# Performance work log

Measured on AMD Instinct MI355X. Metric: run time of the kernel, lower is better.

## Reference

```python
import jax
import jax.numpy as jnp
from jax import lax
import numpy as np

B, ND, H, W = 8, 8, 512, 512
CONF = 0.9
MARGIN = 3.0
MIN_CLUSTER = 50
MAX_X = 102.4
MPP0, MPP1 = 0.2, 0.2
K = 32  # max clusters (torch version grows an unbounded python list)


def setup_inputs() -> dict:
    key = jax.random.key(0)
    k1, k2, k3, k4, k5, k6 = jax.random.split(key, 6)
    return {
        "seg": jax.random.uniform(k1, (B, 1, H, W), dtype=jnp.float32),
        "embedding": jax.random.normal(k2, (B, ND, H, W), dtype=jnp.float32),
        "offset_pred": jax.random.normal(k3, (B, 1, H, W), dtype=jnp.float32),
        "z_pred": jax.random.normal(k4, (B, 1, H, W), dtype=jnp.float32),
        "intrinsic": jax.random.normal(k5, (B, 3, 3), dtype=jnp.float32),
        "extrinsic": jax.random.normal(k6, (B, 4, 4), dtype=jnp.float32),
    }


def _cluster_one(seg_flat, emb_flat):
    # seg_flat: [N], emb_flat: [N, ND]. Greedy sequential embedding clustering
    # (naive_cluster_nd): running-mean centers, assign to nearest center if
    # within MARGIN else open a new one. Fixed K slots; counts>0 marks active.
    nd = emb_flat.shape[1]

    def step(carry, xs):
        centers, counts = carry  # [K, nd], [K]
        s, e = xs
        valid = s >= CONF
        d = jnp.sqrt(jnp.sum((centers - e) ** 2, axis=1))
        d = jnp.where(counts > 0, d, jnp.inf)
        cid_min = jnp.argmin(d).astype(jnp.int32)
        join = d[cid_min] < MARGIN
        n_active = jnp.sum(counts > 0).astype(jnp.int32)
        cid = jnp.where(join, cid_min, jnp.minimum(n_active, K - 1))
        cnt = counts[cid]
        new_c = jnp.where(join, (centers[cid] * cnt + e) / (cnt + 1.0), e)
        centers = jnp.where(valid, centers.at[cid].set(new_c), centers)
        counts = jnp.where(valid, counts.at[cid].add(1.0), counts)
        return (centers, counts), jnp.where(valid, cid, -1)

    init = (jnp.zeros((K, nd), emb_flat.dtype), jnp.zeros((K,), emb_flat.dtype))
    (_, _), cids = lax.scan(step, init, (seg_flat, emb_flat))
    return cids  # [N] int32, -1 = background


def reference(seg, embedding, offset_pred, z_pred, intrinsic, extrinsic):
    b, nd, h, w = embedding.shape
    seg_flat = seg[:, 0].reshape(b, h * w)
    emb_flat = embedding.reshape(b, nd, h * w).transpose(0, 2, 1)  # [B, N, nd]
    cids = jax.vmap(_cluster_one)(seg_flat, emb_flat).reshape(b, h, w)
    lanes = jnp.where(cids >= 0, cids + 1, 0)  # [B, H, W], 0 = background

    # mean_col_by_row_with_offset_z: per (batch, lane, row) mean of col+offset and z
    offset_y = jax.nn.sigmoid(offset_pred[:, 0])          # [B, H, W]
    x_adj = jnp.arange(w, dtype=seg.dtype)[None, None, :] + offset_y
    zc = z_pred[:, 0]
    b_idx = jnp.arange(b)[:, None, None]
    h_idx = jnp.arange(h)[None, :, None]
    seg_ids = ((b_idx * (K + 1) + lanes) * h + h_idx).reshape(-1)
    num = b * (K + 1) * h

    def ssum(v):
        return jax.ops.segment_sum(v.reshape(-1), seg_ids, num_segments=num).reshape(b, K + 1, h)[:, 1:]

    cnt = ssum(jnp.ones((b, h, w), seg.dtype))            # [B, K, H]
    mean_x = ssum(x_adj) / jnp.maximum(cnt, 1.0)
    mean_z = ssum(zc) / jnp.maximum(cnt, 1.0)

    size = cnt.sum(-1)                                    # cluster pixel count
    n_rows = (cnt > 0).sum(-1)                            # rows per lane
    valid = (cnt > 0) & (size[:, :, None] >= MIN_CLUSTER) & (n_rows[:, :, None] >= 2)

    # ego-coordinate transform from forward()
    x_world = (MAX_X / MPP0 - (jnp.arange(h, dtype=seg.dtype) + 0.5)) * MPP0  # [H]
    x_world = jnp.broadcast_to(x_world, (b, K, h))
    y_world = -(mean_x - (w // 2)) * MPP1
    points = jnp.stack([x_world, y_world, mean_z], axis=1)  # [B, 3, K, H]
    points = jnp.where(valid[:, None], points, 0.0)
    return points, valid
```

## Files before the change

kernel.cpp:

```cpp
#include <hip/hip_runtime.h>

#define HW_ (512 * 512)
#define B_ 8
#define H_ 512
#define W_ 512
#define K_ 32
#define CH_ 16
#define CHPIX_ (HW_ / CH_)

typedef float float2v __attribute__((ext_vector_type(2)));

__global__ void k_count(const float* __restrict__ seg, int* __restrict__ chunkCnt) {
  const int blk = blockIdx.x;
  const int t = threadIdx.x;
  const float4* __restrict__ s4 = (const float4*)(seg + (size_t)blk * CHPIX_) + (size_t)t * 16;
  int cnt = 0;
#pragma unroll
  for (int j = 0; j < 16; ++j) {
    float4 v = s4[j];
    cnt += (v.x >= 0.9f) + (v.y >= 0.9f) + (v.z >= 0.9f) + (v.w >= 0.9f);
  }
  __shared__ int red[256];
  red[t] = cnt;
  __syncthreads();
  for (int off = 128; off > 0; off >>= 1) {
    if (t < off) red[t] += red[t + off];
    __syncthreads();
  }
  if (t == 0) chunkCnt[blk] = red[0];
}

__global__ void k_scan(const int* __restrict__ chunkCnt, int* __restrict__ chunkBase,
                       int* __restrict__ nvalid, int cap) {
  const int t = threadIdx.x;
  if (t < B_ * CH_) {
    const int b = t / CH_, c = t % CH_;
    int base = 0;
    for (int q = 0; q < c; ++q) base += chunkCnt[b * CH_ + q];
    chunkBase[t] = base;
    if (c == CH_ - 1) nvalid[b] = min(base + chunkCnt[t], cap);
  }
}

__global__ void k_fill(const float* __restrict__ seg, const float* __restrict__ emb,
                       const int* __restrict__ chunkBase, unsigned char* __restrict__ lanes,
                       int* __restrict__ idxC, float* __restrict__ embC, int cap) {
  const int blk = blockIdx.x;
  const int b = blk / CH_;
  const int t = threadIdx.x;
  const size_t pixbase = (size_t)blk * CHPIX_ + (size_t)t * 64;
  const float4* __restrict__ s4 = (const float4*)(seg + pixbase);

  int cnt = 0;
#pragma unroll
  for (int j = 0; j < 16; ++j) {
    float4 v = s4[j];
    cnt += (v.x >= 0.9f) + (v.y >= 0.9f) + (v.z >= 0.9f) + (v.w >= 0.9f);
  }
  __shared__ int pre[256];
  pre[t] = cnt;
  __syncthreads();
  for (int off = 1; off < 256; off <<= 1) {
    int mine = pre[t];
    int add = (t >= off) ? pre[t - off] : 0;
    __syncthreads();
    pre[t] = mine + add;
    __syncthreads();
  }
  int w = chunkBase[blk] + pre[t] - cnt;

  uint4 z = {0u, 0u, 0u, 0u};
  uint4* lz = (uint4*)(lanes + pixbase);
  lz[0] = z; lz[1] = z; lz[2] = z; lz[3] = z;

  const float* __restrict__ eb = emb + (size_t)b * 8 * HW_;
  const int pixInB = (int)(pixbase - (size_t)b * HW_);
  for (int j = 0; j < 16; ++j) {
    float4 v = s4[j];
    float sv[4] = {v.x, v.y, v.z, v.w};
#pragma unroll
    for (int q = 0; q < 4; ++q) {
      if (sv[q] >= 0.9f && w < cap) {
        const int p = pixInB + j * 4 + q;
        idxC[(size_t)b * cap + w] = p;
        float* dst = embC + ((size_t)b * cap + w) * 8;
#pragma unroll
        for (int dd = 0; dd < 8; ++dd) dst[dd] = eb[(size_t)dd * HW_ + p];
        ++w;
      }
    }
  }
}


#define TILE_ 32

__device__ __forceinline__ void stage16(const float* g, float* l) {
  __builtin_amdgcn_global_load_lds(
      (const __attribute__((address_space(1))) void*)g,
      (__attribute__((address_space(3))) void*)l, 16, 0, 0);
}

#define RLU(V, L) ((unsigned)__builtin_amdgcn_readlane((int)(V), (L)))
#define PKF(A, B, C) __builtin_elementwise_fma((A), (B), (C))

#define STEPQ(J, US, LS)                                                             \
  do {                                                                               \
    float2v t01 = C01 - e01_##US;                                                    \
    float2v t23 = C23 - e23_##US;                                                    \
    float2v t45 = C45 - e45_##US;                                                    \
    float2v t67 = C67 - e67_##US;                                                    \
    float2v p = t01 * t01;                                                           \
    p = PKF(t23, t23, p);                                                            \
    p = PKF(t45, t45, p);                                                            \
    p = PKF(t67, t67, p);                                                            \
    float dsq = p.x + p.y;                                                           \
    unsigned db = __float_as_uint(dsq);                                              \
    unsigned dbm = db > emptyBits ? db : emptyBits;         \
    unsigned mn = (dbm & 0xFFFFFFE0u) | (unsigned)cl;                                \
    unsigned mr;                                                                     \
    mr = (unsigned)__builtin_amdgcn_update_dpp(0, (int)mn, 0xB1, 0xF, 0xF, true);    \
    mn = mn < mr ? mn : mr;                                                          \
    mr = (unsigned)__builtin_amdgcn_update_dpp(0, (int)mn, 0x4E, 0xF, 0xF, true);    \
    mn = mn < mr ? mn : mr;                                                          \
    mr = (unsigned)__builtin_amdgcn_update_dpp(0, (int)mn, 0x141, 0xF, 0xF, true);   \
    mn = mn < mr ? mn : mr;                                                          \
    mr = (unsigned)__builtin_amdgcn_update_dpp(0, (int)mn, 0x140, 0xF, 0xF, true);   \
    mn = mn < mr ? mn : mr;                                                          \
    unsigned q0 = RLU(mn, 0), q1 = RLU(mn, 16);                                      \
    unsigned mv = q0 < q1 ? q0 : q1;                            \
    bool join = mv < 0x41100000u;            \
    int cid = join ? (int)(mv & 31u) : (nact < 31 ? nact : 31);                      \
    nact += join ? 0 : 1;                                                            \
    bool own = (cl == cid);                                                          \
    float wj = join ? inv : 1.0f;                                                    \
    float w = own ? wj : 0.0f;                                                       \
    float2v wv = {w, w};                                                             \
    C01 = PKF(t01, -wv, C01);                                          \
    C23 = PKF(t23, -wv, C23);                                                        \
    C45 = PKF(t45, -wv, C45);                                                        \
    C67 = PKF(t67, -wv, C67);                                                        \
    cnt += own ? 1.0f : 0.0f;                                                        \
    inv = __builtin_amdgcn_rcpf(cnt + 1.0f);          \
    emptyBits = own ? 0u : emptyBits;                                                \
    pk |= (unsigned long long)(unsigned)(cid + 1) << (((J) & 7) * 8);                \
    if (((J) & 7) == 7) {                                                            \
      if (lane == 0) *(unsigned long long*)(cptr + ((J) & ~7)) = pk;                 \
      pk = 0ULL;                                                                     \
    }                                                                                \
    if ((J) < TILE_ - 2) {       \
      e01_##LS = ebq[((J) + 2) * 4 + 0];                                             \
      e23_##LS = ebq[((J) + 2) * 4 + 1];                                             \
      e45_##LS = ebq[((J) + 2) * 4 + 2];                                             \
      e67_##LS = ebq[((J) + 2) * 4 + 3];                                             \
    }                                                                                \
  } while (0)

__global__ __launch_bounds__(64, 1) void k_cluster(const float* __restrict__ embC,
                                                   const int* __restrict__ nvalid,
                                                   unsigned char* __restrict__ cidArr,
                                                   int cap) {
  __shared__ float lds[512];
  const int b = blockIdx.x;
  const int lane = threadIdx.x;
  const int cl = lane & 31;
  const int n = nvalid[b];
  if (n <= 0) return;
  const int nTiles = (n + TILE_ - 1) / TILE_;

  const float* src = embC + (size_t)b * cap * 8 + lane * 4;
  unsigned char* cidB = cidArr + (size_t)b * HW_;

  float2v C01 = {0.f, 0.f}, C23 = C01, C45 = C01, C67 = C01;
  float2v e01_0, e23_0, e45_0, e67_0;
  float2v e01_1, e23_1, e45_1, e67_1;
  float2v e01_2, e23_2, e45_2, e67_2;
  float cnt = 0.f, inv = 1.0f;
  unsigned emptyBits = 0x7F800000u;
  int nact = 0;
  unsigned long long pk = 0ULL;

  stage16(src, lds);
  asm volatile("s_waitcnt vmcnt(0)" ::: "memory");
  __builtin_amdgcn_sched_barrier(0);

  for (int ti = 0; ti < nTiles; ++ti) {
    const bool more = (ti + 1 < nTiles);
    const float2v* ebq = (const float2v*)((const char*)lds + (ti & 1) * 1024);
    unsigned char* cptr = cidB + ti * TILE_;

    e01_0 = ebq[0]; e23_0 = ebq[1]; e45_0 = ebq[2]; e67_0 = ebq[3];
    e01_1 = ebq[4]; e23_1 = ebq[5]; e45_1 = ebq[6]; e67_1 = ebq[7];

    if (more)
      stage16(src + (size_t)(ti + 1) * 256, lds + ((ti + 1) & 1) * 256);

    STEPQ(0, 0, 2);  STEPQ(1, 1, 0);  STEPQ(2, 2, 1);  STEPQ(3, 0, 2);
    STEPQ(4, 1, 0);  STEPQ(5, 2, 1);  STEPQ(6, 0, 2);  STEPQ(7, 1, 0);
    STEPQ(8, 2, 1);  STEPQ(9, 0, 2);  STEPQ(10, 1, 0); STEPQ(11, 2, 1);
    STEPQ(12, 0, 2); STEPQ(13, 1, 0); STEPQ(14, 2, 1); STEPQ(15, 0, 2);
    STEPQ(16, 1, 0); STEPQ(17, 2, 1); STEPQ(18, 0, 2); STEPQ(19, 1, 0);
    STEPQ(20, 2, 1); STEPQ(21, 0, 2); STEPQ(22, 1, 0); STEPQ(23, 2, 1);
    STEPQ(24, 0, 2); STEPQ(25, 1, 0); STEPQ(26, 2, 1); STEPQ(27, 0, 2);
    STEPQ(28, 1, 0); STEPQ(29, 2, 1); STEPQ(30, 0, 2); STEPQ(31, 1, 0);

    if (more) {
      asm volatile("s_waitcnt vmcnt(4)" ::: "memory");
      __builtin_amdgcn_sched_barrier(0);
    }
  }
}

__global__ void k_scatter(const unsigned char* __restrict__ cidArr,
                          const int* __restrict__ idxC, const int* __restrict__ nvalid,
                          unsigned char* __restrict__ lanes, int cap) {
  const int b = blockIdx.y;
  const int n = nvalid[b];
  for (int j = blockIdx.x * blockDim.x + threadIdx.x; j < n; j += gridDim.x * blockDim.x) {
    lanes[(size_t)b * HW_ + idxC[(size_t)b * cap + j]] = cidArr[(size_t)b * HW_ + j];
  }
}

__global__ void k_rowsum(const unsigned char* __restrict__ lanes,
                         const float* __restrict__ offp, const float* __restrict__ zp,
                         float* __restrict__ cnt, float* __restrict__ sx,
                         float* __restrict__ sz) {
  const int bh = blockIdx.x;
  const int b = bh >> 9, h = bh & 511;
  __shared__ float sc[33], sxx[33], szz[33];
  const int t = threadIdx.x;
  if (t < 33) { sc[t] = 0.f; sxx[t] = 0.f; szz[t] = 0.f; }
  __syncthreads();
  const size_t base = (size_t)bh * W_;
  for (int x = t; x < W_; x += 256) {
    int ln = lanes[base + x];
    float o = offp[base + x];
    float sig = 1.0f / (1.0f + expf(-o));
    float xa = (float)x + sig;
    float zv = zp[base + x];
    atomicAdd(&sc[ln], 1.0f);
    atomicAdd(&sxx[ln], xa);
    atomicAdd(&szz[ln], zv);
  }
  __syncthreads();
  if (t >= 1 && t < 33) {
    size_t o = ((size_t)b * K_ + (t - 1)) * H_ + h;
    cnt[o] = sc[t]; sx[o] = sxx[t]; sz[o] = szz[t];
  }
}

__global__ void k_final(const float* __restrict__ cnt, const float* __restrict__ sx,
                        const float* __restrict__ sz, float* __restrict__ out) {
  const int bk = blockIdx.x;
  const int b = bk >> 5, k = bk & 31;
  const int h = threadIdx.x;
  const size_t o = (size_t)bk * H_ + h;
  float c = cnt[o];
  float sc_ = c, sn = (c > 0.f) ? 1.f : 0.f;
#pragma unroll
  for (int off = 32; off >= 1; off >>= 1) {
    sc_ += __shfl_down(sc_, off);
    sn += __shfl_down(sn, off);
  }
  __shared__ float rs[8], rn[8], tot[2];
  const int wid = h >> 6, lid = h & 63;
  if (lid == 0) { rs[wid] = sc_; rn[wid] = sn; }
  __syncthreads();
  if (h == 0) {
    float a = 0, bb = 0;
#pragma unroll
    for (int q = 0; q < 8; ++q) { a += rs[q]; bb += rn[q]; }
    tot[0] = a; tot[1] = bb;
  }
  __syncthreads();
  float size = tot[0], nrows = tot[1];
  bool valid = (c > 0.f) && (size >= 50.f) && (nrows >= 2.f);
  float mx = sx[o] / fmaxf(c, 1.f);
  float mz = sz[o] / fmaxf(c, 1.f);
  float xw = (512.0f - ((float)h + 0.5f)) * 0.2f;
  float yw = -(mx - 256.0f) * 0.2f;
  out[((size_t)(b * 3 + 0) * K_ + k) * H_ + h] = valid ? xw : 0.f;
  out[((size_t)(b * 3 + 1) * K_ + k) * H_ + h] = valid ? yw : 0.f;
  out[((size_t)(b * 3 + 2) * K_ + k) * H_ + h] = valid ? mz : 0.f;
  out[(size_t)B_ * 3 * K_ * H_ + (size_t)bk * H_ + h] = valid ? 1.f : 0.f;
}

extern "C" void kernel_launch(void* const* d_in, const int* in_sizes, int n_in,
                              void* d_out, int out_size, void* d_ws, size_t ws_size,
                              hipStream_t stream) {
  const float* seg  = (const float*)d_in[0];
  const float* emb  = (const float*)d_in[1];
  const float* offp = (const float*)d_in[2];
  const float* zp   = (const float*)d_in[3];
  float* out = (float*)d_out;
  char* ws = (char*)d_ws;

  const size_t lanesOff = 0;
  const size_t cntOff   = (size_t)B_ * HW_;
  const size_t sxOff    = cntOff + (size_t)B_ * K_ * H_ * 4;
  const size_t szOff    = sxOff  + (size_t)B_ * K_ * H_ * 4;
  const size_t nvOff    = szOff  + (size_t)B_ * K_ * H_ * 4;
  const size_t ccOff    = nvOff + 256;
  const size_t cbOff    = ccOff + 1024;
  const size_t cidOff   = cbOff + 1024;
  const size_t idxOff   = cidOff + (size_t)B_ * HW_;
  size_t avail = (ws_size > idxOff + 8192) ? (ws_size - idxOff - 8192) : 0;
  long long capLL = (long long)(avail / ((size_t)B_ * 36));
  if (capLL > (long long)HW_) capLL = HW_;
  if (capLL < 2) capLL = 2;
  capLL &= ~1LL;
  const int cap = (int)capLL;
  const size_t embOff = idxOff + (size_t)B_ * cap * 4;

  unsigned char* lanes = (unsigned char*)(ws + lanesOff);
  float* cnt = (float*)(ws + cntOff);
  float* sx  = (float*)(ws + sxOff);
  float* sz  = (float*)(ws + szOff);
  int* nvalid = (int*)(ws + nvOff);
  int* chunkCnt  = (int*)(ws + ccOff);
  int* chunkBase = (int*)(ws + cbOff);
  unsigned char* cidArr = (unsigned char*)(ws + cidOff);
  int* idxC   = (int*)(ws + idxOff);
  float* embC = (float*)(ws + embOff);

  k_count<<<B_ * CH_, 256, 0, stream>>>(seg, chunkCnt);
  k_scan<<<1, 128, 0, stream>>>(chunkCnt, chunkBase, nvalid, cap);
  k_fill<<<B_ * CH_, 256, 0, stream>>>(seg, emb, chunkBase, lanes, idxC, embC, cap);
  k_cluster<<<B_, 64, 0, stream>>>(embC, nvalid, cidArr, cap);
  k_scatter<<<dim3(64, B_), 256, 0, stream>>>(cidArr, idxC, nvalid, lanes, cap);
  k_rowsum<<<B_ * H_, 256, 0, stream>>>(lanes, offp, zp, cnt, sx, sz);
  k_final<<<B_ * K_, H_, 0, stream>>>(cnt, sx, sz, out);
}
```

Baseline: 3.035 ms.

## Pack four batches per wave in sequential clustering, two centers per lane

The clustering kernel now handles four batch elements per 64-lane wave. Each 16-lane row owns one batch, and each lane holds two cluster centers packed in float2 pairs. The argmin reduction stays inside a DPP row, so the readlane steps drop out of the per-pixel serial dependency chain. k_fill writes each embedding value twice, making 16 floats per pixel to match the packed layout, and workspace capacity is recomputed for that size. In exchange the compacted buffer doubles, each step does more vector arithmetic, every wave runs to the longest of its four batches, and only two workgroups are launched instead of eight.

```diff
diff --git a/kernel.cpp b/kernel.cpp
--- a/kernel.cpp
+++ b/kernel.cpp
@@ -83,9 +83,13 @@
       if (sv[q] >= 0.9f && w < cap) {
         const int p = pixInB + j * 4 + q;
         idxC[(size_t)b * cap + w] = p;
-        float* dst = embC + ((size_t)b * cap + w) * 8;
-#pragma unroll
-        for (int dd = 0; dd < 8; ++dd) dst[dd] = eb[(size_t)dd * HW_ + p];
+        float* dst = embC + ((size_t)b * cap + w) * 16;
+#pragma unroll
+        for (int dd = 0; dd < 8; ++dd) {
+          float vv = eb[(size_t)dd * HW_ + p];
+          dst[2 * dd] = vv;
+          dst[2 * dd + 1] = vv;
+        }
         ++w;
       }
     }
@@ -101,23 +105,36 @@
       (__attribute__((address_space(3))) void*)l, 16, 0, 0);
 }
 
-#define RLU(V, L) ((unsigned)__builtin_amdgcn_readlane((int)(V), (L)))
 #define PKF(A, B, C) __builtin_elementwise_fma((A), (B), (C))
+
+#define LOADSLOT(LS, EB, P)                                    \
+  s##LS##a = *(const float4*)((EB) + (P) * 64);                \
+  s##LS##b = *(const float4*)((EB) + (P) * 64 + 16);           \
+  s##LS##c = *(const float4*)((EB) + (P) * 64 + 32);           \
+  s##LS##d = *(const float4*)((EB) + (P) * 64 + 48);
 
 #define STEPQ(J, US, LS)                                                             \
   do {                                                                               \
-    float2v t01 = C01 - e01_##US;                                                    \
-    float2v t23 = C23 - e23_##US;                                                    \
-    float2v t45 = C45 - e45_##US;                                                    \
-    float2v t67 = C67 - e67_##US;                                                    \
-    float2v p = t01 * t01;                                                           \
-    p = PKF(t23, t23, p);                                                            \
-    p = PKF(t45, t45, p);                                                            \
-    p = PKF(t67, t67, p);                                                            \
-    float dsq = p.x + p.y;                                                           \
-    unsigned db = __float_as_uint(dsq);                                              \
-    unsigned dbm = db > emptyBits ? db : emptyBits;         \
-    unsigned mn = (dbm & 0xFFFFFFE0u) | (unsigned)cl;                                \
+    float2v e0 = {s##US##a.x, s##US##a.y}, e1 = {s##US##a.z, s##US##a.w};            \
+    float2v e2 = {s##US##b.x, s##US##b.y}, e3 = {s##US##b.z, s##US##b.w};            \
+    float2v e4 = {s##US##c.x, s##US##c.y}, e5 = {s##US##c.z, s##US##c.w};            \
+    float2v e6 = {s##US##d.x, s##US##d.y}, e7 = {s##US##d.z, s##US##d.w};            \
+    float2v t0 = C0 - e0, t1 = C1 - e1, t2 = C2 - e2, t3 = C3 - e3;                  \
+    float2v t4 = C4 - e4, t5 = C5 - e5, t6 = C6 - e6, t7 = C7 - e7;                  \
+    float2v pa = t0 * t0; pa = PKF(t1, t1, pa);                                      \
+    float2v pb = t2 * t2; pb = PKF(t3, t3, pb);                                      \
+    float2v pc = t4 * t4; pc = PKF(t5, t5, pc);                                      \
+    float2v pd = t6 * t6; pd = PKF(t7, t7, pd);                                      \
+    pa = pa + pb;                                                                    \
+    pc = pc + pd;                                                                    \
+    pa = pa + pc;                                             \
+    unsigned dL = __float_as_uint(pa.x);                                             \
+    unsigned dH = __float_as_uint(pa.y);                                             \
+    dL = dL > emL ? dL : emL;                          \
+    dH = dH > emH ? dH : emH;                                                        \
+    unsigned kL = (dL & 0xFFFFFFE0u) | idL;                                          \
+    unsigned kH = (dH & 0xFFFFFFE0u) | idH;                                          \
+    unsigned mn = kL < kH ? kL : kH;                                                 \
     unsigned mr;                                                                     \
     mr = (unsigned)__builtin_amdgcn_update_dpp(0, (int)mn, 0xB1, 0xF, 0xF, true);    \
     mn = mn < mr ? mn : mr;                                                          \
@@ -126,74 +143,95 @@
     mr = (unsigned)__builtin_amdgcn_update_dpp(0, (int)mn, 0x141, 0xF, 0xF, true);   \
     mn = mn < mr ? mn : mr;                                                          \
     mr = (unsigned)__builtin_amdgcn_update_dpp(0, (int)mn, 0x140, 0xF, 0xF, true);   \
-    mn = mn < mr ? mn : mr;                                                          \
-    unsigned q0 = RLU(mn, 0), q1 = RLU(mn, 16);                                      \
-    unsigned mv = q0 < q1 ? q0 : q1;                            \
-    bool join = mv < 0x41100000u;            \
-    int cid = join ? (int)(mv & 31u) : (nact < 31 ? nact : 31);                      \
-    nact += join ? 0 : 1;                                                            \
-    bool own = (cl == cid);                                                          \
-    float wj = join ? inv : 1.0f;                                                    \
-    float w = own ? wj : 0.0f;                                                       \
-    float2v wv = {w, w};                                                             \
-    C01 = PKF(t01, -wv, C01);                                          \
-    C23 = PKF(t23, -wv, C23);                                                        \
-    C45 = PKF(t45, -wv, C45);                                                        \
-    C67 = PKF(t67, -wv, C67);                                                        \
-    cnt += own ? 1.0f : 0.0f;                                                        \
-    inv = __builtin_amdgcn_rcpf(cnt + 1.0f);          \
-    emptyBits = own ? 0u : emptyBits;                                                \
-    pk |= (unsigned long long)(unsigned)(cid + 1) << (((J) & 7) * 8);                \
+    mn = mn < mr ? mn : mr;              \
+    bool join = mn < 0x41100000u;            \
+    unsigned nactc = nactv < 31u ? nactv : 31u;                                      \
+    float wLj = (kL == mn) ? inv2.x : 0.0f;                                          \
+    float wHj = (kH == mn) ? inv2.y : 0.0f;                                          \
+    float wLn = (idL == nactc) ? 1.0f : 0.0f;                                        \
+    float wHn = (idH == nactc) ? 1.0f : 0.0f;                                        \
+    float wL = join ? wLj : wLn;                                                     \
+    float wH = join ? wHj : wHn;                                                     \
+    float2v w2 = {wL, wH};                                                           \
+    C0 = PKF(t0, -w2, C0);                                             \
+    C1 = PKF(t1, -w2, C1);                                                           \
+    C2 = PKF(t2, -w2, C2);                                                           \
+    C3 = PKF(t3, -w2, C3);                                                           \
+    C4 = PKF(t4, -w2, C4);                                                           \
+    C5 = PKF(t5, -w2, C5);                                                           \
+    C6 = PKF(t6, -w2, C6);                                                           \
+    C7 = PKF(t7, -w2, C7);                                                           \
+    float2v ownf = {(wL > 0.0f) ? 1.0f : 0.0f, (wH > 0.0f) ? 1.0f : 0.0f};           \
+    cnt2 = cnt2 + ownf;                                                              \
+    float2v cp1 = cnt2 + one2;                                                       \
+    inv2.x = __builtin_amdgcn_rcpf(cp1.x);            \
+    inv2.y = __builtin_amdgcn_rcpf(cp1.y);                                           \
+    emL = (wL > 0.0f) ? 0u : emL;                                                    \
+    emH = (wH > 0.0f) ? 0u : emH;                                                    \
+    nactv += join ? 0u : 1u;                                                         \
+    unsigned cid = join ? (mn & 31u) : nactc;                                        \
+    pk |= (unsigned long long)(cid + 1u) << (((J) & 7) * 8);                         \
     if (((J) & 7) == 7) {                                                            \
-      if (lane == 0) *(unsigned long long*)(cptr + ((J) & ~7)) = pk;                 \
+      if (q16 == 0) *(unsigned long long*)(cpG + ((J) & ~7)) = pk;                   \
       pk = 0ULL;                                                                     \
     }                                                                                \
-    if ((J) < TILE_ - 2) {       \
-      e01_##LS = ebq[((J) + 2) * 4 + 0];                                             \
-      e23_##LS = ebq[((J) + 2) * 4 + 1];                                             \
-      e45_##LS = ebq[((J) + 2) * 4 + 2];                                             \
-      e67_##LS = ebq[((J) + 2) * 4 + 3];                                             \
-    }                                                                                \
+    if ((J) < TILE_ - 2) { LOADSLOT(LS, ebase, (J) + 2) }                            \
   } while (0)
 
 __global__ __launch_bounds__(64, 1) void k_cluster(const float* __restrict__ embC,
                                                    const int* __restrict__ nvalid,
                                                    unsigned char* __restrict__ cidArr,
                                                    int cap) {
-  __shared__ float lds[512];
-  const int b = blockIdx.x;
+  __shared__ float lds[4160];
+  const int blk = blockIdx.x;
   const int lane = threadIdx.x;
-  const int cl = lane & 31;
-  const int n = nvalid[b];
-  if (n <= 0) return;
-  const int nTiles = (n + TILE_ - 1) / TILE_;
-
-  const float* src = embC + (size_t)b * cap * 8 + lane * 4;
-  unsigned char* cidB = cidArr + (size_t)b * HW_;
-
-  float2v C01 = {0.f, 0.f}, C23 = C01, C45 = C01, C67 = C01;
-  float2v e01_0, e23_0, e45_0, e67_0;
-  float2v e01_1, e23_1, e45_1, e67_1;
-  float2v e01_2, e23_2, e45_2, e67_2;
-  float cnt = 0.f, inv = 1.0f;
-  unsigned emptyBits = 0x7F800000u;
-  int nact = 0;
+  const int q16 = lane & 15;
+  const int g = lane >> 4;
+  const int bBase = blk * 4;
+  const int n0 = nvalid[bBase], n1 = nvalid[bBase + 1];
+  const int n2 = nvalid[bBase + 2], n3 = nvalid[bBase + 3];
+  int nMax = n0 > n1 ? n0 : n1;
+  nMax = nMax > n2 ? nMax : n2;
+  nMax = nMax > n3 ? nMax : n3;
+  if (nMax <= 0) return;
+  const int nTiles = (nMax + TILE_ - 1) / TILE_;
+
+  unsigned char* cpBase = cidArr + (size_t)(bBase + g) * HW_;
+
+  float2v C0 = {0.f, 0.f}, C1 = C0, C2 = C0, C3 = C0, C4 = C0, C5 = C0, C6 = C0, C7 = C0;
+  float2v cnt2 = {0.f, 0.f}, inv2 = {1.f, 1.f};
+  const float2v one2 = {1.f, 1.f};
+  unsigned emL = 0x7F800000u, emH = 0x7F800000u;
+  const unsigned idL = (unsigned)q16, idH = (unsigned)q16 + 16u;
+  unsigned nactv = 0u;
   unsigned long long pk = 0ULL;
-
-  stage16(src, lds);
+  float4 s0a, s0b, s0c, s0d, s1a, s1b, s1c, s1d, s2a, s2b, s2c, s2d;
+
+  for (int bb = 0; bb < 4; ++bb) {
+    const float* s = embC + (size_t)(bBase + bb) * cap * 16 + (size_t)lane * 4;
+    stage16(s, lds + bb * 520);
+    stage16(s + 256, lds + bb * 520 + 256);
+  }
   asm volatile("s_waitcnt vmcnt(0)" ::: "memory");
   __builtin_amdgcn_sched_barrier(0);
 
   for (int ti = 0; ti < nTiles; ++ti) {
     const bool more = (ti + 1 < nTiles);
-    const float2v* ebq = (const float2v*)((const char*)lds + (ti & 1) * 1024);
-    unsigned char* cptr = cidB + ti * TILE_;
-
-    e01_0 = ebq[0]; e23_0 = ebq[1]; e45_0 = ebq[2]; e67_0 = ebq[3];
-    e01_1 = ebq[4]; e23_1 = ebq[5]; e45_1 = ebq[6]; e67_1 = ebq[7];
-
-    if (more)
-      stage16(src + (size_t)(ti + 1) * 256, lds + ((ti + 1) & 1) * 256);
+    const char* ebase = (const char*)lds + (ti & 1) * 8320 + g * 2080;
+    unsigned char* cpG = cpBase + ti * TILE_;
+
+    LOADSLOT(0, ebase, 0)
+    LOADSLOT(1, ebase, 1)
+
+    if (more) {
+      const int ph = ((ti + 1) & 1) * 2080;
+      for (int bb = 0; bb < 4; ++bb) {
+        const float* s = embC + (size_t)(bBase + bb) * cap * 16 +
+                         (size_t)(ti + 1) * 512 + (size_t)lane * 4;
+        stage16(s, lds + ph + bb * 520);
+        stage16(s + 256, lds + ph + bb * 520 + 256);
+      }
+    }
 
     STEPQ(0, 0, 2);  STEPQ(1, 1, 0);  STEPQ(2, 2, 1);  STEPQ(3, 0, 2);
     STEPQ(4, 1, 0);  STEPQ(5, 2, 1);  STEPQ(6, 0, 2);  STEPQ(7, 1, 0);
@@ -304,8 +342,8 @@
   const size_t cbOff    = ccOff + 1024;
   const size_t cidOff   = cbOff + 1024;
   const size_t idxOff   = cidOff + (size_t)B_ * HW_;
-  size_t avail = (ws_size > idxOff + 8192) ? (ws_size - idxOff - 8192) : 0;
-  long long capLL = (long long)(avail / ((size_t)B_ * 36));
+  size_t avail = (ws_size > idxOff + 16384) ? (ws_size - idxOff - 16384) : 0;
+  long long capLL = (long long)(avail / ((size_t)B_ * 68));
   if (capLL > (long long)HW_) capLL = HW_;
   if (capLL < 2) capLL = 2;
   capLL &= ~1LL;
@@ -326,7 +364,7 @@
   k_count<<<B_ * CH_, 256, 0, stream>>>(seg, chunkCnt);
   k_scan<<<1, 128, 0, stream>>>(chunkCnt, chunkBase, nvalid, cap);
   k_fill<<<B_ * CH_, 256, 0, stream>>>(seg, emb, chunkBase, lanes, idxC, embC, cap);
-  k_cluster<<<B_, 64, 0, stream>>>(embC, nvalid, cidArr, cap);
+  k_cluster<<<B_ / 4, 64, 0, stream>>>(embC, nvalid, cidArr, cap);
   k_scatter<<<dim3(64, B_), 256, 0, stream>>>(cidArr, idxC, nvalid, lanes, cap);
   k_rowsum<<<B_ * H_, 256, 0, stream>>>(lanes, offp, zp, cnt, sx, sz);
   k_final<<<B_ * K_, H_, 0, stream>>>(cnt, sx, sz, out);
```

Result: slower. 4.320 ms (+42.3%).
